# Performance work log

Hardware: AMD Instinct MI355X
Metric: run time of the kernel (lower is better)

## Reference

```python
import jax, jax.numpy as jnp
import numpy as np

K = 3  # TAGConv default number of hops
N, E = 50000, 800000
F_X, F_POS, HID, OUT = 6, 2, 64, 10


def _tagconv(x, W, b, src, dst, norm, n):
    # TAGConv: out = sum_{k=0}^{K} (A_norm^k x) @ W[k] + b
    out = x @ W[0]
    h = x
    for k in range(1, K + 1):
        # one propagate step: gather from src, weight, scatter-sum to dst
        h = jax.ops.segment_sum(norm[:, None] * h[src], dst, num_segments=n)
        out = out + h @ W[k]
    return out + b


def setup_inputs() -> dict:
    key = jax.random.key(0)
    ks = jax.random.split(key, 12)
    x = jax.random.normal(ks[0], (N, F_X), dtype=jnp.float32)
    pos = jax.random.normal(ks[1], (N, F_POS), dtype=jnp.float32)
    edge_index = jax.random.randint(ks[2], (2, E), 0, N, dtype=jnp.int64)
    edge_attr = jax.random.uniform(ks[3], (E,), dtype=jnp.float32)
    s = 0.1
    W1 = jax.random.normal(ks[4], (K + 1, F_X + F_POS, HID), dtype=jnp.float32) * s
    b1 = jnp.zeros((HID,), dtype=jnp.float32)
    W2 = jax.random.normal(ks[5], (K + 1, HID, HID), dtype=jnp.float32) * s
    b2 = jnp.zeros((HID,), dtype=jnp.float32)
    W3 = jax.random.normal(ks[6], (K + 1, HID, OUT), dtype=jnp.float32) * s
    b3 = jnp.zeros((OUT,), dtype=jnp.float32)
    return {"x": x, "pos": pos, "edge_attr": edge_attr,
            "W1": W1, "b1": b1, "W2": W2, "b2": b2, "W3": W3, "b3": b3,
            "edge_index": edge_index}


def reference(x, pos, edge_attr, W1, b1, W2, b2, W3, b3, edge_index):
    n = x.shape[0]
    src, dst = edge_index[0], edge_index[1]
    # gcn_norm (no self loops, as in TAGConv): deg over destination (col)
    deg = jax.ops.segment_sum(edge_attr, dst, num_segments=n)
    dinv = jnp.where(deg > 0, jax.lax.rsqrt(deg), jnp.zeros_like(deg))
    norm = dinv[src] * edge_attr * dinv[dst]
    h = jnp.concatenate([x, pos], axis=1)
    h = jax.nn.relu(_tagconv(h, W1, b1, src, dst, norm, n))
    # F.dropout with training=False is identity (eval reference)
    h = jax.nn.relu(_tagconv(h, W2, b2, src, dst, norm, n))
    h = _tagconv(h, W3, b3, src, dst, norm, n)
    return jax.nn.log_softmax(h, axis=1)
```

## Files before the change

### kernel.cpp

```cpp
#include <hip/hip_runtime.h>
#include <math.h>


#define NN 50000
#define EE 800000
#define HID 64
#define NOUT 10
#define CH 512

#define NB 391
#define CAP 2400
#define K1_EPB 2048

typedef __attribute__((ext_vector_type(8))) short bf16x8;
typedef __attribute__((ext_vector_type(4))) float f32x4;

__device__ __forceinline__ unsigned bf16rnd(float x) {
    unsigned u = __float_as_uint(x);
    return (u + 0x7FFFu + ((u >> 16) & 1u)) >> 16;
}
__device__ __forceinline__ unsigned packbf2(float a, float b) {
    return bf16rnd(a) | (bf16rnd(b) << 16);
}
__device__ __forceinline__ float bflo(unsigned u) { return __uint_as_float(u << 16); }
__device__ __forceinline__ float bfhi(unsigned u) { return __uint_as_float(u & 0xFFFF0000u); }

__global__ __launch_bounds__(512) void bucket_scatter_kernel(
        const int* __restrict__ src, const int* __restrict__ dst,
        const float* __restrict__ ea, int* __restrict__ cursor,
        int2* __restrict__ regions, int e) {
    __shared__ int hist[NB];
    __shared__ int base_s[NB];
    int tid = threadIdx.x;
    int e0 = blockIdx.x * K1_EPB;
    int e1 = e0 + K1_EPB; if (e1 > e) e1 = e;
    int d[4], s[4];
    float w[4];
    int cnt = 0;
    for (int i = e0 + tid; i < e1; i += 512) {
        d[cnt] = dst[i]; s[cnt] = src[i]; w[cnt] = ea[i];
        ++cnt;
    }
    for (int i = tid; i < NB; i += 512) hist[i] = 0;
    __syncthreads();
    for (int j = 0; j < cnt; ++j)
        atomicAdd(&hist[d[j] >> 7], 1);
    __syncthreads();
    for (int b = tid; b < NB; b += 512) {
        int c = hist[b];
        base_s[b] = (c > 0) ? atomicAdd(&cursor[b], c) : 0;
        hist[b] = 0;
    }
    __syncthreads();
    for (int j = 0; j < cnt; ++j) {
        int b = d[j] >> 7;
        int r = atomicAdd(&hist[b], 1);
        int pos = base_s[b] + r;
        if (pos < CAP)
            regions[(size_t)b * CAP + pos] =
                make_int2(((d[j] & 127) << 16) | s[j], __float_as_int(w[j]));
    }
}

__global__ __launch_bounds__(512) void bucket_build_kernel(
        const int* __restrict__ cursor, int2* __restrict__ regions,
        float* __restrict__ dinv, int* __restrict__ row_start, int n) {
    __shared__ int2 rec[CAP];
    __shared__ int hist[128];
    __shared__ float easum[128];
    __shared__ float dl[128];
    __shared__ int off[129];
    __shared__ int lcur[128];
    int b = blockIdx.x;
    int tid = threadIdx.x;
    int cnt = cursor[b]; if (cnt > CAP) cnt = CAP;
    size_t rb = (size_t)b * CAP;
    if (tid < 128) { hist[tid] = 0; easum[tid] = 0.f; lcur[tid] = 0; }
    __syncthreads();
    for (int i = tid; i < cnt; i += 512) {
        int2 r = regions[rb + i];
        rec[i] = r;
        int f = r.x >> 16;
        atomicAdd(&hist[f], 1);
        atomicAdd(&easum[f], __int_as_float(r.y));
    }
    __syncthreads();
    if (tid < 128) {
        int lane = tid & 63;
        int v = hist[tid];
        for (int o2 = 1; o2 < 64; o2 <<= 1) {
            int y = __shfl_up(v, o2, 64);
            if (lane >= o2) v += y;
        }
        off[tid + 1] = v;
        float s2 = easum[tid];
        dl[tid] = (s2 > 0.f) ? rsqrtf(s2) : 0.f;
    }
    __syncthreads();
    if (tid == 255) off[0] = 0;
    if (tid >= 64 && tid < 128) off[tid + 1] += off[64];
    __syncthreads();
    if (tid < 128) {
        int node = b * 128 + tid;
        if (node <= n) row_start[node] = b * CAP + off[tid];
        if (node < n)  dinv[node] = dl[tid];
    }
    __syncthreads();
    for (int i = tid; i < cnt; i += 512) {
        int2 r = rec[i];
        int f = r.x >> 16;
        int s = r.x & 0xFFFF;
        int p = atomicAdd(&lcur[f], 1);
        float w0 = __int_as_float(r.y) * dl[f];
        regions[rb + off[f] + p] = make_int2(s, __float_as_int(w0));
    }
}

__global__ __launch_bounds__(256) void pack1_kernel(const float* __restrict__ x,
                                                    const float* __restrict__ pos,
                                                    unsigned short* __restrict__ B1, int n) {
    int i = blockIdx.x * blockDim.x + threadIdx.x;
    if (i >= n) return;
    float2 a = *reinterpret_cast<const float2*>(x + (size_t)i * 6);
    float2 b = *reinterpret_cast<const float2*>(x + (size_t)i * 6 + 2);
    float2 c = *reinterpret_cast<const float2*>(x + (size_t)i * 6 + 4);
    float2 p = *reinterpret_cast<const float2*>(pos + (size_t)i * 2);
    uint4 o;
    o.x = packbf2(a.x, a.y);
    o.y = packbf2(b.x, b.y);
    o.z = packbf2(c.x, c.y);
    o.w = packbf2(p.x, p.y);
    *reinterpret_cast<uint4*>(B1 + (size_t)i * 32) = o;
}

template <int SCALE>
__global__ __launch_bounds__(256) void prop8b_kernel(const int* __restrict__ row_start,
                                                     const int* __restrict__ cursor,
                                                     int2* __restrict__ edges,
                                                     const float* __restrict__ dinv,
                                                     const unsigned short* __restrict__ Gin,
                                                     unsigned short* __restrict__ Gout, int n) {
    constexpr int TEAM = 8, NPB = 32;
    __shared__ int2 se[CH];
    int tid = threadIdx.x;
    int nb = blockIdx.x * NPB;
    int node = nb + tid / TEAM;
    int es = tid % TEAM;
    int nbEnd = (nb + NPB < n) ? (nb + NPB) : n;
    int bkt = nb >> 7;
    int cc = cursor[bkt]; if (cc > CAP) cc = CAP;
    int ce = bkt * CAP + cc;
    int blkBeg = row_start[nb];
    int blkEnd = row_start[nbEnd]; if (blkEnd > ce) blkEnd = ce;
    int beg = 0, end = 0;
    if (node < n) {
        beg = row_start[node];
        end = row_start[node + 1]; if (end > ce) end = ce;
    }
    float a0 = 0.f, a1 = 0.f, a2 = 0.f, a3 = 0.f, a4 = 0.f, a5 = 0.f, a6 = 0.f, a7 = 0.f;
    for (int base = blkBeg; base < blkEnd; base += CH) {
        int m = blkEnd - base; if (m > CH) m = CH;
        __syncthreads();
        for (int i = tid; i < m; i += 256) {
            int2 r = edges[base + i];
            if (SCALE) {
                r.y = __float_as_int(__int_as_float(r.y) * dinv[r.x]);
                edges[base + i] = r;
            }
            se[i] = r;
        }
        __syncthreads();
        int lo = (beg > base) ? (beg - base) : 0;
        int hi = ((end < base + m) ? end : (base + m)) - base;
        for (int i = lo + es; i < hi; i += TEAM) {
            int2 e = se[i];
            float w = __int_as_float(e.y);
            const uint4 v = *reinterpret_cast<const uint4*>(Gin + (size_t)e.x * 32);
            a0 += w * bflo(v.x); a1 += w * bfhi(v.x);
            a2 += w * bflo(v.y); a3 += w * bfhi(v.y);
            a4 += w * bflo(v.z); a5 += w * bfhi(v.z);
            a6 += w * bflo(v.w); a7 += w * bfhi(v.w);
        }
    }
    #pragma unroll
    for (int msk = 1; msk < TEAM; msk <<= 1) {
        a0 += __shfl_xor(a0, msk); a1 += __shfl_xor(a1, msk);
        a2 += __shfl_xor(a2, msk); a3 += __shfl_xor(a3, msk);
        a4 += __shfl_xor(a4, msk); a5 += __shfl_xor(a5, msk);
        a6 += __shfl_xor(a6, msk); a7 += __shfl_xor(a7, msk);
    }
    if (node < n && es == 0) {
        uint4 o;
        o.x = packbf2(a0, a1);
        o.y = packbf2(a2, a3);
        o.z = packbf2(a4, a5);
        o.w = packbf2(a6, a7);
        *reinterpret_cast<uint4*>(Gout + (size_t)node * 32) = o;
    }
}

template <int TPN, int ES, bool ACC>
__global__ __launch_bounds__(256) void prop_kernel(const int* __restrict__ row_start,
                                                   const int* __restrict__ cursor,
                                                   const int2* __restrict__ edges,
                                                   const float* __restrict__ hin, int in_stride,
                                                   float* __restrict__ hout, int out_stride, int n) {
    constexpr int TEAM = TPN * ES;
    constexpr int NPB = 256 / TEAM;
    __shared__ int2 se[CH];
    int tid = threadIdx.x;
    int nb = blockIdx.x * NPB;
    int node = nb + tid / TEAM;
    int t = tid % TEAM;
    int es = t / TPN;
    int lane = t % TPN;
    int nbEnd = (nb + NPB < n) ? (nb + NPB) : n;
    int bkt = nb >> 7;
    int cc = cursor[bkt]; if (cc > CAP) cc = CAP;
    int ce = bkt * CAP + cc;
    int blkBeg = row_start[nb];
    int blkEnd = row_start[nbEnd]; if (blkEnd > ce) blkEnd = ce;
    int beg = 0, end = 0;
    if (node < n) {
        beg = row_start[node];
        end = row_start[node + 1]; if (end > ce) end = ce;
    }
    float ax = 0.f, ay = 0.f, az = 0.f, aw = 0.f;
    for (int base = blkBeg; base < blkEnd; base += CH) {
        int m = blkEnd - base; if (m > CH) m = CH;
        __syncthreads();
        for (int i = tid; i < m; i += 256) se[i] = edges[base + i];
        __syncthreads();
        int lo = (beg > base) ? (beg - base) : 0;
        int hi = ((end < base + m) ? end : (base + m)) - base;
        for (int i = lo + es; i < hi; i += ES) {
            int2 e = se[i];
            float w = __int_as_float(e.y);
            const float4 v = *reinterpret_cast<const float4*>(hin + (size_t)e.x * in_stride + lane * 4);
            ax += w * v.x; ay += w * v.y; az += w * v.z; aw += w * v.w;
        }
    }
    #pragma unroll
    for (int msk = TPN; msk < TEAM; msk <<= 1) {
        ax += __shfl_xor(ax, msk);
        ay += __shfl_xor(ay, msk);
        az += __shfl_xor(az, msk);
        aw += __shfl_xor(aw, msk);
    }
    if (node < n && es == 0) {
        float4* po = reinterpret_cast<float4*>(hout + (size_t)node * out_stride + lane * 4);
        float4 r = make_float4(ax, ay, az, aw);
        if (ACC) { float4 o = *po; r.x += o.x; r.y += o.y; r.z += o.z; r.w += o.w; }
        *po = r;
    }
}

__global__ __launch_bounds__(256) void prop64b_kernel(const int* __restrict__ row_start,
                                                      const int* __restrict__ cursor,
                                                      const int2* __restrict__ edges,
                                                      const unsigned short* __restrict__ Gin,
                                                      unsigned short* __restrict__ Gout, int n) {
    constexpr int TPN = 8, ES = 4, TEAM = 32, NPB = 8;
    __shared__ int2 se[CH];
    int tid = threadIdx.x;
    int nb = blockIdx.x * NPB;
    int node = nb + tid / TEAM;
    int t = tid % TEAM;
    int es = t / TPN;
    int lane = t % TPN;
    int nbEnd = (nb + NPB < n) ? (nb + NPB) : n;
    int bkt = nb >> 7;
    int cc = cursor[bkt]; if (cc > CAP) cc = CAP;
    int ce = bkt * CAP + cc;
    int blkBeg = row_start[nb];
    int blkEnd = row_start[nbEnd]; if (blkEnd > ce) blkEnd = ce;
    int beg = 0, end = 0;
    if (node < n) {
        beg = row_start[node];
        end = row_start[node + 1]; if (end > ce) end = ce;
    }
    float a0 = 0.f, a1 = 0.f, a2 = 0.f, a3 = 0.f, a4 = 0.f, a5 = 0.f, a6 = 0.f, a7 = 0.f;
    for (int base = blkBeg; base < blkEnd; base += CH) {
        int m = blkEnd - base; if (m > CH) m = CH;
        __syncthreads();
        for (int i = tid; i < m; i += 256) se[i] = edges[base + i];
        __syncthreads();
        int lo = (beg > base) ? (beg - base) : 0;
        int hi = ((end < base + m) ? end : (base + m)) - base;
        for (int i = lo + es; i < hi; i += ES) {
            int2 e = se[i];
            float w = __int_as_float(e.y);
            const uint4 v = *reinterpret_cast<const uint4*>(Gin + (size_t)e.x * 256 + lane * 8);
            a0 += w * bflo(v.x); a1 += w * bfhi(v.x);
            a2 += w * bflo(v.y); a3 += w * bfhi(v.y);
            a4 += w * bflo(v.z); a5 += w * bfhi(v.z);
            a6 += w * bflo(v.w); a7 += w * bfhi(v.w);
        }
    }
    #pragma unroll
    for (int msk = TPN; msk < TEAM; msk <<= 1) {
        a0 += __shfl_xor(a0, msk); a1 += __shfl_xor(a1, msk);
        a2 += __shfl_xor(a2, msk); a3 += __shfl_xor(a3, msk);
        a4 += __shfl_xor(a4, msk); a5 += __shfl_xor(a5, msk);
        a6 += __shfl_xor(a6, msk); a7 += __shfl_xor(a7, msk);
    }
    if (node < n && es == 0) {
        uint4 o;
        o.x = packbf2(a0, a1);
        o.y = packbf2(a2, a3);
        o.z = packbf2(a4, a5);
        o.w = packbf2(a6, a7);
        *reinterpret_cast<uint4*>(Gout + (size_t)node * 256 + lane * 8) = o;
    }
}

__global__ __launch_bounds__(256) void prop_final_kernel(const int* __restrict__ row_start,
                                                         const int* __restrict__ cursor,
                                                         const int2* __restrict__ edges,
                                                         const float* __restrict__ hin,
                                                         const float* __restrict__ g0,
                                                         const float* __restrict__ b3,
                                                         float* __restrict__ out, int n) {
    constexpr int TPN = 4, ES = 2, TEAM = 8, NPB = 32;
    __shared__ int2 se[CH];
    int tid = threadIdx.x;
    int nb = blockIdx.x * NPB;
    int node = nb + tid / TEAM;
    int t = tid % TEAM;
    int es = t / TPN;
    int lane = t % TPN;
    int nbEnd = (nb + NPB < n) ? (nb + NPB) : n;
    int bkt = nb >> 7;
    int cc = cursor[bkt]; if (cc > CAP) cc = CAP;
    int ce = bkt * CAP + cc;
    int blkBeg = row_start[nb];
    int blkEnd = row_start[nbEnd]; if (blkEnd > ce) blkEnd = ce;
    int beg = 0, end = 0;
    if (node < n) {
        beg = row_start[node];
        end = row_start[node + 1]; if (end > ce) end = ce;
    }
    float ax = 0.f, ay = 0.f, az = 0.f, aw = 0.f;
    for (int base = blkBeg; base < blkEnd; base += CH) {
        int m = blkEnd - base; if (m > CH) m = CH;
        __syncthreads();
        for (int i = tid; i < m; i += 256) se[i] = edges[base + i];
        __syncthreads();
        int lo = (beg > base) ? (beg - base) : 0;
        int hi = ((end < base + m) ? end : (base + m)) - base;
        for (int i = lo + es; i < hi; i += ES) {
            int2 e = se[i];
            float w = __int_as_float(e.y);
            const float4 v = *reinterpret_cast<const float4*>(hin + (size_t)e.x * 64 + lane * 4);
            ax += w * v.x; ay += w * v.y; az += w * v.z; aw += w * v.w;
        }
    }
    ax += __shfl_xor(ax, TPN);
    ay += __shfl_xor(ay, TPN);
    az += __shfl_xor(az, TPN);
    aw += __shfl_xor(aw, TPN);
    if (node < n && es == 0) {
        const float4 g = *reinterpret_cast<const float4*>(g0 + (size_t)node * 64 + lane * 4);
        float vv[4] = {ax + g.x, ay + g.y, az + g.z, aw + g.w};
        int c0 = lane * 4;
        float mloc = -1e30f;
        #pragma unroll
        for (int c = 0; c < 4; ++c) {
            int col = c0 + c;
            if (col < NOUT) { vv[c] += b3[col]; mloc = fmaxf(mloc, vv[c]); }
        }
        float mo = fmaxf(mloc, __shfl_xor(mloc, 1));
        mo = fmaxf(mo, __shfl_xor(mo, 2));
        float sl = 0.f;
        #pragma unroll
        for (int c = 0; c < 4; ++c) {
            int col = c0 + c;
            if (col < NOUT) sl += __expf(vv[c] - mo);
        }
        sl += __shfl_xor(sl, 1);
        sl += __shfl_xor(sl, 2);
        float ls = __logf(sl);
        #pragma unroll
        for (int c = 0; c < 4; ++c) {
            int col = c0 + c;
            if (col < NOUT) out[(size_t)node * NOUT + col] = vv[c] - mo - ls;
        }
    }
}

__global__ __launch_bounds__(256) void mm1_kernel(const unsigned short* __restrict__ B1,
                                                  const float* __restrict__ W1,
                                                  const float* __restrict__ b1,
                                                  unsigned short* __restrict__ G, int n) {
    __shared__ unsigned short w1s[2048];
    __shared__ unsigned short hs[64 * 64];
    int tid = threadIdx.x;
    int wave = tid >> 6;
    int lane = tid & 63;
    int nodeBase = blockIdx.x * 64;

    {
        int l = tid & 63;
        int t = tid >> 6;
        int k0 = (l >> 4) << 3;
        int col = t * 16 + (l & 15);
        unsigned short tmp[8];
        #pragma unroll
        for (int j = 0; j < 8; ++j)
            tmp[j] = (unsigned short)bf16rnd(W1[(size_t)(k0 + j) * 64 + col]);
        *reinterpret_cast<uint4*>(w1s + tid * 8) = *reinterpret_cast<const uint4*>(tmp);
    }
    __syncthreads();

    int arow = nodeBase + wave * 16 + (lane & 15);
    bf16x8 a = {};
    if (arow < n)
        a = *reinterpret_cast<const bf16x8*>(B1 + (size_t)arow * 32 + ((lane >> 4) << 3));
    const unsigned short* wb = w1s + lane * 8;
    f32x4 acc0 = {0.f, 0.f, 0.f, 0.f}, acc1 = {0.f, 0.f, 0.f, 0.f};
    f32x4 acc2 = {0.f, 0.f, 0.f, 0.f}, acc3 = {0.f, 0.f, 0.f, 0.f};
    acc0 = __builtin_amdgcn_mfma_f32_16x16x32_bf16(a, *reinterpret_cast<const bf16x8*>(wb),        acc0, 0, 0, 0);
    acc1 = __builtin_amdgcn_mfma_f32_16x16x32_bf16(a, *reinterpret_cast<const bf16x8*>(wb + 512),  acc1, 0, 0, 0);
    acc2 = __builtin_amdgcn_mfma_f32_16x16x32_bf16(a, *reinterpret_cast<const bf16x8*>(wb + 1024), acc2, 0, 0, 0);
    acc3 = __builtin_amdgcn_mfma_f32_16x16x32_bf16(a, *reinterpret_cast<const bf16x8*>(wb + 1536), acc3, 0, 0, 0);

    {
        int c = lane & 15;
        int rbase = wave * 16 + (lane >> 4) * 4;
        f32x4 accs[4] = {acc0, acc1, acc2, acc3};
        #pragma unroll
        for (int t = 0; t < 4; ++t) {
            int col = t * 16 + c;
            float bb = b1[col];
            #pragma unroll
            for (int r = 0; r < 4; ++r) {
                float v = accs[t][r] + bb;
                hs[(rbase + r) * 64 + col] = (unsigned short)bf16rnd(v > 0.f ? v : 0.f);
            }
        }
    }
    __syncthreads();
    for (int i = tid; i < 512; i += 256) {
        int nd = i >> 3, ch = i & 7;
        int node = nodeBase + nd;
        if (node < n)
            *reinterpret_cast<uint4*>(G + (size_t)node * 256 + ch * 8) =
                *reinterpret_cast<const uint4*>(hs + nd * 64 + ch * 8);
    }
}

__global__ __launch_bounds__(256) void mm23_kernel(const unsigned short* __restrict__ G,
                                                   const float* __restrict__ W2,
                                                   const float* __restrict__ b2,
                                                   const float* __restrict__ W3,
                                                   float* __restrict__ T, int n) {
    constexpr int HP = 68;
    __shared__ __align__(16) char smem[33792];
    unsigned short* w2s = (unsigned short*)smem;
    float* HsT = (float*)smem;
    float* Ws  = (float*)(smem + 64 * HP * 4);
    int tid = threadIdx.x;
    int wave = tid >> 6;
    int lane = tid & 63;
    int nodeBase = blockIdx.x * 64;

    for (int slot = tid; slot < 2048; slot += 256) {
        int l = slot & 63;
        int s = (slot >> 6) & 7;
        int t = slot >> 9;
        int k0 = s * 32 + ((l >> 4) << 3);
        int col = t * 16 + (l & 15);
        unsigned short tmp[8];
        #pragma unroll
        for (int j = 0; j < 8; ++j)
            tmp[j] = (unsigned short)bf16rnd(W2[(size_t)(k0 + j) * 64 + col]);
        *reinterpret_cast<uint4*>(w2s + slot * 8) = *reinterpret_cast<const uint4*>(tmp);
    }
    __syncthreads();

    int arow = nodeBase + wave * 16 + (lane & 15);
    bool aval = (arow < n);
    const unsigned short* arp = G + (size_t)arow * 256 + ((lane >> 4) << 3);
    f32x4 acc0 = {0.f, 0.f, 0.f, 0.f}, acc1 = {0.f, 0.f, 0.f, 0.f};
    f32x4 acc2 = {0.f, 0.f, 0.f, 0.f}, acc3 = {0.f, 0.f, 0.f, 0.f};
    #pragma unroll
    for (int s = 0; s < 8; ++s) {
        bf16x8 a = {};
        if (aval) a = *reinterpret_cast<const bf16x8*>(arp + s * 32);
        const unsigned short* wb = w2s + ((size_t)s * 64 + lane) * 8;
        bf16x8 bf0 = *reinterpret_cast<const bf16x8*>(wb);
        bf16x8 bf1 = *reinterpret_cast<const bf16x8*>(wb + 4096);
        bf16x8 bf2 = *reinterpret_cast<const bf16x8*>(wb + 8192);
        bf16x8 bf3 = *reinterpret_cast<const bf16x8*>(wb + 12288);
        acc0 = __builtin_amdgcn_mfma_f32_16x16x32_bf16(a, bf0, acc0, 0, 0, 0);
        acc1 = __builtin_amdgcn_mfma_f32_16x16x32_bf16(a, bf1, acc1, 0, 0, 0);
        acc2 = __builtin_amdgcn_mfma_f32_16x16x32_bf16(a, bf2, acc2, 0, 0, 0);
        acc3 = __builtin_amdgcn_mfma_f32_16x16x32_bf16(a, bf3, acc3, 0, 0, 0);
    }
    __syncthreads();

    {
        int c = lane & 15;
        int rbase = wave * 16 + (lane >> 4) * 4;
        f32x4 accs[4] = {acc0, acc1, acc2, acc3};
        #pragma unroll
        for (int t = 0; t < 4; ++t) {
            int col = t * 16 + c;
            float bb = b2[col];
            #pragma unroll
            for (int r = 0; r < 4; ++r) {
                float v = accs[t][r] + bb;
                HsT[col * HP + rbase + r] = v > 0.f ? v : 0.f;
            }
        }
    }
    for (int i = tid; i < 64 * 64; i += 256) {
        int r = i >> 6, c2 = i & 63;
        int k = c2 >> 4, j = c2 & 15;
        Ws[i] = (j < NOUT) ? W3[((size_t)k * 64 + r) * NOUT + j] : 0.f;
    }
    __syncthreads();

    int ndq = tid >> 4;
    int f4  = tid & 15;
    float4 t0 = make_float4(0.f, 0.f, 0.f, 0.f);
    float4 t1 = make_float4(0.f, 0.f, 0.f, 0.f);
    float4 t2 = make_float4(0.f, 0.f, 0.f, 0.f);
    float4 t3 = make_float4(0.f, 0.f, 0.f, 0.f);
    #pragma unroll 8
    for (int k = 0; k < 64; ++k) {
        const float4 hq = *reinterpret_cast<const float4*>(&HsT[k * HP + ndq * 4]);
        const float4 wq = *reinterpret_cast<const float4*>(&Ws[k * 64 + f4 * 4]);
        t0.x += hq.x * wq.x; t0.y += hq.x * wq.y; t0.z += hq.x * wq.z; t0.w += hq.x * wq.w;
        t1.x += hq.y * wq.x; t1.y += hq.y * wq.y; t1.z += hq.y * wq.z; t1.w += hq.y * wq.w;
        t2.x += hq.z * wq.x; t2.y += hq.z * wq.y; t2.z += hq.z * wq.z; t2.w += hq.z * wq.w;
        t3.x += hq.w * wq.x; t3.y += hq.w * wq.y; t3.z += hq.w * wq.z; t3.w += hq.w * wq.w;
    }
    float4 ts[4] = {t0, t1, t2, t3};
    #pragma unroll
    for (int i = 0; i < 4; ++i) {
        int node = nodeBase + ndq * 4 + i;
        if (node < n)
            *reinterpret_cast<float4*>(T + (size_t)node * 64 + f4 * 4) = ts[i];
    }
}

extern "C" void kernel_launch(void* const* d_in, const int* in_sizes, int n_in,
                              void* d_out, int out_size, void* d_ws, size_t ws_size,
                              hipStream_t stream) {
    const float* x   = (const float*)d_in[0];
    const float* pos = (const float*)d_in[1];
    const float* ea  = (const float*)d_in[2];
    const float* W1  = (const float*)d_in[3];
    const float* b1  = (const float*)d_in[4];
    const float* W2  = (const float*)d_in[5];
    const float* b2  = (const float*)d_in[6];
    const float* W3  = (const float*)d_in[7];
    const float* b3  = (const float*)d_in[8];
    const int* eidx  = (const int*)d_in[9];
    const int* src = eidx;
    const int* dst = eidx + EE;
    float* outp = (float*)d_out;

    size_t off = 0;
    char* base = (char*)d_ws;
    auto alloc = [&](size_t bytes) -> void* {
        void* p = base + off;
        off += (bytes + 255) & ~(size_t)255;
        return p;
    };
    int*   cursor    = (int*)alloc(NB * 4);
    int*   row_start = (int*)alloc((NN + 1) * 4);
    float* dinv      = (float*)alloc(NN * 4);
    int2*  edges     = (int2*)alloc((size_t)NB * CAP * 8);
    unsigned short* G  = (unsigned short*)alloc((size_t)NN * 256 * 2);
    unsigned short* B1 = (unsigned short*)alloc((size_t)NN * 32 * 2);
    float* T         = (float*)alloc((size_t)NN * 64 * 4);
    (void)ws_size;

    const int B = 256;
    const int gN = (NN + B - 1) / B;
    const int gK1 = (EE + K1_EPB - 1) / K1_EPB;
    const int gMM2 = (NN + 63) / 64;
    const int gP32 = (NN + 31) / 32;
    const int gP8  = (NN + 7) / 8;

    hipMemsetAsync(cursor, 0, NB * 4, stream);

    bucket_scatter_kernel<<<gK1, 512, 0, stream>>>(src, dst, ea, cursor, edges, EE);
    bucket_build_kernel<<<NB, 512, 0, stream>>>(cursor, edges, dinv, row_start, NN);

    pack1_kernel<<<gN, B, 0, stream>>>(x, pos, B1, NN);
    prop8b_kernel<1><<<gP32, B, 0, stream>>>(row_start, cursor, edges, dinv, B1,      B1 + 8,  NN);
    prop8b_kernel<0><<<gP32, B, 0, stream>>>(row_start, cursor, edges, dinv, B1 + 8,  B1 + 16, NN);
    prop8b_kernel<0><<<gP32, B, 0, stream>>>(row_start, cursor, edges, dinv, B1 + 16, B1 + 24, NN);
    mm1_kernel<<<gMM2, B, 0, stream>>>(B1, W1, b1, G, NN);

    prop64b_kernel<<<gP8, B, 0, stream>>>(row_start, cursor, edges, G,       G + 64,  NN);
    prop64b_kernel<<<gP8, B, 0, stream>>>(row_start, cursor, edges, G + 64,  G + 128, NN);
    prop64b_kernel<<<gP8, B, 0, stream>>>(row_start, cursor, edges, G + 128, G + 192, NN);
    mm23_kernel<<<gMM2, B, 0, stream>>>(G, W2, b2, W3, T, NN);

    prop_kernel<4, 2, true><<<gP32, B, 0, stream>>>(row_start, cursor, edges, T + 48, 64, T + 32, 64, NN);
    prop_kernel<4, 2, true><<<gP32, B, 0, stream>>>(row_start, cursor, edges, T + 32, 64, T + 16, 64, NN);
    prop_final_kernel<<<gP32, B, 0, stream>>>(row_start, cursor, edges, T + 16, T, b3, outp, NN);
}
```

Baseline: 273.7 us.

## Compress edge records to 32-bit (16-bit src + fp16 weight) and retune propagation teams

Edge records change from int2 (src, fp32 weight) to a packed 32-bit word holding a 16-bit source index and an fp16 weight, written to a separate buffer by the build kernel. This halves edge-list traffic in all nine propagation passes and lets the shared-memory chunk size double to 1024. The 10-wide propagation kernels switch to 4 edge-slices per node with 16 nodes per block. The cost is reduced weight precision from fp16 rounding, including the rescaled weights in the first pass. The 16-bit index also only works because N is below 65536.

```diff
diff --git a/kernel.cpp b/kernel.cpp
--- a/kernel.cpp
+++ b/kernel.cpp
@@ -1,4 +1,5 @@
 #include <hip/hip_runtime.h>
+#include <hip/hip_fp16.h>
 #include <math.h>
 
 
@@ -6,7 +7,7 @@
 #define EE 800000
 #define HID 64
 #define NOUT 10
-#define CH 512
+#define CH 1024
 
 #define NB 391
 #define CAP 2400
@@ -24,6 +25,15 @@
 }
 __device__ __forceinline__ float bflo(unsigned u) { return __uint_as_float(u << 16); }
 __device__ __forceinline__ float bfhi(unsigned u) { return __uint_as_float(u & 0xFFFF0000u); }
+__device__ __forceinline__ unsigned f16b(float x) {
+    __half h = __float2half_rn(x);
+    return (unsigned)*reinterpret_cast<unsigned short*>(&h);
+}
+__device__ __forceinline__ float f16f(unsigned u) {
+    unsigned short us = (unsigned short)u;
+    __half h = *reinterpret_cast<__half*>(&us);
+    return __half2float(h);
+}
 
 __global__ __launch_bounds__(512) void bucket_scatter_kernel(
         const int* __restrict__ src, const int* __restrict__ dst,
@@ -63,7 +73,8 @@
 }
 
 __global__ __launch_bounds__(512) void bucket_build_kernel(
-        const int* __restrict__ cursor, int2* __restrict__ regions,
+        const int* __restrict__ cursor, const int2* __restrict__ regions,
+        unsigned* __restrict__ erec,
         float* __restrict__ dinv, int* __restrict__ row_start, int n) {
     __shared__ int2 rec[CAP];
     __shared__ int hist[128];
@@ -109,10 +120,10 @@
     for (int i = tid; i < cnt; i += 512) {
         int2 r = rec[i];
         int f = r.x >> 16;
-        int s = r.x & 0xFFFF;
+        unsigned s = (unsigned)(r.x & 0xFFFF);
         int p = atomicAdd(&lcur[f], 1);
         float w0 = __int_as_float(r.y) * dl[f];
-        regions[rb + off[f] + p] = make_int2(s, __float_as_int(w0));
+        erec[rb + off[f] + p] = s | (f16b(w0) << 16);
     }
 }
 
@@ -136,12 +147,12 @@
 template <int SCALE>
 __global__ __launch_bounds__(256) void prop8b_kernel(const int* __restrict__ row_start,
                                                      const int* __restrict__ cursor,
-                                                     int2* __restrict__ edges,
+                                                     unsigned* __restrict__ erec,
                                                      const float* __restrict__ dinv,
                                                      const unsigned short* __restrict__ Gin,
                                                      unsigned short* __restrict__ Gout, int n) {
     constexpr int TEAM = 8, NPB = 32;
-    __shared__ int2 se[CH];
+    __shared__ unsigned se[CH];
     int tid = threadIdx.x;
     int nb = blockIdx.x * NPB;
     int node = nb + tid / TEAM;
@@ -162,10 +173,11 @@
         int m = blkEnd - base; if (m > CH) m = CH;
         __syncthreads();
         for (int i = tid; i < m; i += 256) {
-            int2 r = edges[base + i];
+            unsigned r = erec[base + i];
             if (SCALE) {
-                r.y = __float_as_int(__int_as_float(r.y) * dinv[r.x]);
-                edges[base + i] = r;
+                float w = f16f(r >> 16) * dinv[r & 0xFFFF];
+                r = (r & 0xFFFFu) | (f16b(w) << 16);
+                erec[base + i] = r;
             }
             se[i] = r;
         }
@@ -173,9 +185,9 @@
         int lo = (beg > base) ? (beg - base) : 0;
         int hi = ((end < base + m) ? end : (base + m)) - base;
         for (int i = lo + es; i < hi; i += TEAM) {
-            int2 e = se[i];
-            float w = __int_as_float(e.y);
-            const uint4 v = *reinterpret_cast<const uint4*>(Gin + (size_t)e.x * 32);
+            unsigned e = se[i];
+            float w = f16f(e >> 16);
+            const uint4 v = *reinterpret_cast<const uint4*>(Gin + (size_t)(e & 0xFFFF) * 32);
             a0 += w * bflo(v.x); a1 += w * bfhi(v.x);
             a2 += w * bflo(v.y); a3 += w * bfhi(v.y);
             a4 += w * bflo(v.z); a5 += w * bfhi(v.z);
@@ -202,12 +214,12 @@
 template <int TPN, int ES, bool ACC>
 __global__ __launch_bounds__(256) void prop_kernel(const int* __restrict__ row_start,
                                                    const int* __restrict__ cursor,
-                                                   const int2* __restrict__ edges,
+                                                   const unsigned* __restrict__ erec,
                                                    const float* __restrict__ hin, int in_stride,
                                                    float* __restrict__ hout, int out_stride, int n) {
     constexpr int TEAM = TPN * ES;
     constexpr int NPB = 256 / TEAM;
-    __shared__ int2 se[CH];
+    __shared__ unsigned se[CH];
     int tid = threadIdx.x;
     int nb = blockIdx.x * NPB;
     int node = nb + tid / TEAM;
@@ -229,14 +241,14 @@
     for (int base = blkBeg; base < blkEnd; base += CH) {
         int m = blkEnd - base; if (m > CH) m = CH;
         __syncthreads();
-        for (int i = tid; i < m; i += 256) se[i] = edges[base + i];
+        for (int i = tid; i < m; i += 256) se[i] = erec[base + i];
         __syncthreads();
         int lo = (beg > base) ? (beg - base) : 0;
         int hi = ((end < base + m) ? end : (base + m)) - base;
         for (int i = lo + es; i < hi; i += ES) {
-            int2 e = se[i];
-            float w = __int_as_float(e.y);
-            const float4 v = *reinterpret_cast<const float4*>(hin + (size_t)e.x * in_stride + lane * 4);
+            unsigned e = se[i];
+            float w = f16f(e >> 16);
+            const float4 v = *reinterpret_cast<const float4*>(hin + (size_t)(e & 0xFFFF) * in_stride + lane * 4);
             ax += w * v.x; ay += w * v.y; az += w * v.z; aw += w * v.w;
         }
     }
@@ -257,11 +269,11 @@
 
 __global__ __launch_bounds__(256) void prop64b_kernel(const int* __restrict__ row_start,
                                                       const int* __restrict__ cursor,
-                                                      const int2* __restrict__ edges,
+                                                      const unsigned* __restrict__ erec,
                                                       const unsigned short* __restrict__ Gin,
                                                       unsigned short* __restrict__ Gout, int n) {
     constexpr int TPN = 8, ES = 4, TEAM = 32, NPB = 8;
-    __shared__ int2 se[CH];
+    __shared__ unsigned se[CH];
     int tid = threadIdx.x;
     int nb = blockIdx.x * NPB;
     int node = nb + tid / TEAM;
@@ -283,14 +295,14 @@
     for (int base = blkBeg; base < blkEnd; base += CH) {
         int m = blkEnd - base; if (m > CH) m = CH;
         __syncthreads();
-        for (int i = tid; i < m; i += 256) se[i] = edges[base + i];
+        for (int i = tid; i < m; i += 256) se[i] = erec[base + i];
         __syncthreads();
         int lo = (beg > base) ? (beg - base) : 0;
         int hi = ((end < base + m) ? end : (base + m)) - base;
         for (int i = lo + es; i < hi; i += ES) {
-            int2 e = se[i];
-            float w = __int_as_float(e.y);
-            const uint4 v = *reinterpret_cast<const uint4*>(Gin + (size_t)e.x * 256 + lane * 8);
+            unsigned e = se[i];
+            float w = f16f(e >> 16);
+            const uint4 v = *reinterpret_cast<const uint4*>(Gin + (size_t)(e & 0xFFFF) * 256 + lane * 8);
             a0 += w * bflo(v.x); a1 += w * bfhi(v.x);
             a2 += w * bflo(v.y); a3 += w * bfhi(v.y);
             a4 += w * bflo(v.z); a5 += w * bfhi(v.z);
@@ -316,13 +328,13 @@
 
 __global__ __launch_bounds__(256) void prop_final_kernel(const int* __restrict__ row_start,
                                                          const int* __restrict__ cursor,
-                                                         const int2* __restrict__ edges,
+                                                         const unsigned* __restrict__ erec,
                                                          const float* __restrict__ hin,
                                                          const float* __restrict__ g0,
                                                          const float* __restrict__ b3,
                                                          float* __restrict__ out, int n) {
-    constexpr int TPN = 4, ES = 2, TEAM = 8, NPB = 32;
-    __shared__ int2 se[CH];
+    constexpr int TPN = 4, ES = 4, TEAM = 16, NPB = 16;
+    __shared__ unsigned se[CH];
     int tid = threadIdx.x;
     int nb = blockIdx.x * NPB;
     int node = nb + tid / TEAM;
@@ -344,21 +356,24 @@
     for (int base = blkBeg; base < blkEnd; base += CH) {
         int m = blkEnd - base; if (m > CH) m = CH;
         __syncthreads();
-        for (int i = tid; i < m; i += 256) se[i] = edges[base + i];
+        for (int i = tid; i < m; i += 256) se[i] = erec[base + i];
         __syncthreads();
         int lo = (beg > base) ? (beg - base) : 0;
         int hi = ((end < base + m) ? end : (base + m)) - base;
         for (int i = lo + es; i < hi; i += ES) {
-            int2 e = se[i];
-            float w = __int_as_float(e.y);
-            const float4 v = *reinterpret_cast<const float4*>(hin + (size_t)e.x * 64 + lane * 4);
+            unsigned e = se[i];
+            float w = f16f(e >> 16);
+            const float4 v = *reinterpret_cast<const float4*>(hin + (size_t)(e & 0xFFFF) * 64 + lane * 4);
             ax += w * v.x; ay += w * v.y; az += w * v.z; aw += w * v.w;
         }
     }
-    ax += __shfl_xor(ax, TPN);
-    ay += __shfl_xor(ay, TPN);
-    az += __shfl_xor(az, TPN);
-    aw += __shfl_xor(aw, TPN);
+    #pragma unroll
+    for (int msk = TPN; msk < TEAM; msk <<= 1) {
+        ax += __shfl_xor(ax, msk);
+        ay += __shfl_xor(ay, msk);
+        az += __shfl_xor(az, msk);
+        aw += __shfl_xor(aw, msk);
+    }
     if (node < n && es == 0) {
         const float4 g = *reinterpret_cast<const float4*>(g0 + (size_t)node * 64 + lane * 4);
         float vv[4] = {ax + g.x, ay + g.y, az + g.z, aw + g.w};
@@ -572,7 +587,8 @@
     int*   cursor    = (int*)alloc(NB * 4);
     int*   row_start = (int*)alloc((NN + 1) * 4);
     float* dinv      = (float*)alloc(NN * 4);
-    int2*  edges     = (int2*)alloc((size_t)NB * CAP * 8);
+    int2*  regions   = (int2*)alloc((size_t)NB * CAP * 8);
+    unsigned* erec   = (unsigned*)alloc((size_t)NB * CAP * 4);
     unsigned short* G  = (unsigned short*)alloc((size_t)NN * 256 * 2);
     unsigned short* B1 = (unsigned short*)alloc((size_t)NN * 32 * 2);
     float* T         = (float*)alloc((size_t)NN * 64 * 4);
@@ -583,25 +599,26 @@
     const int gK1 = (EE + K1_EPB - 1) / K1_EPB;
     const int gMM2 = (NN + 63) / 64;
     const int gP32 = (NN + 31) / 32;
+    const int gP16 = (NN + 15) / 16;
     const int gP8  = (NN + 7) / 8;
 
     hipMemsetAsync(cursor, 0, NB * 4, stream);
 
-    bucket_scatter_kernel<<<gK1, 512, 0, stream>>>(src, dst, ea, cursor, edges, EE);
-    bucket_build_kernel<<<NB, 512, 0, stream>>>(cursor, edges, dinv, row_start, NN);
+    bucket_scatter_kernel<<<gK1, 512, 0, stream>>>(src, dst, ea, cursor, regions, EE);
+    bucket_build_kernel<<<NB, 512, 0, stream>>>(cursor, regions, erec, dinv, row_start, NN);
 
     pack1_kernel<<<gN, B, 0, stream>>>(x, pos, B1, NN);
-    prop8b_kernel<1><<<gP32, B, 0, stream>>>(row_start, cursor, edges, dinv, B1,      B1 + 8,  NN);
-    prop8b_kernel<0><<<gP32, B, 0, stream>>>(row_start, cursor, edges, dinv, B1 + 8,  B1 + 16, NN);
-    prop8b_kernel<0><<<gP32, B, 0, stream>>>(row_start, cursor, edges, dinv, B1 + 16, B1 + 24, NN);
+    prop8b_kernel<1><<<gP32, B, 0, stream>>>(row_start, cursor, erec, dinv, B1,      B1 + 8,  NN);
+    prop8b_kernel<0><<<gP32, B, 0, stream>>>(row_start, cursor, erec, dinv, B1 + 8,  B1 + 16, NN);
+    prop8b_kernel<0><<<gP32, B, 0, stream>>>(row_start, cursor, erec, dinv, B1 + 16, B1 + 24, NN);
     mm1_kernel<<<gMM2, B, 0, stream>>>(B1, W1, b1, G, NN);
 
-    prop64b_kernel<<<gP8, B, 0, stream>>>(row_start, cursor, edges, G,       G + 64,  NN);
-    prop64b_kernel<<<gP8, B, 0, stream>>>(row_start, cursor, edges, G + 64,  G + 128, NN);
-    prop64b_kernel<<<gP8, B, 0, stream>>>(row_start, cursor, edges, G + 128, G + 192, NN);
+    prop64b_kernel<<<gP8, B, 0, stream>>>(row_start, cursor, erec, G,       G + 64,  NN);
+    prop64b_kernel<<<gP8, B, 0, stream>>>(row_start, cursor, erec, G + 64,  G + 128, NN);
+    prop64b_kernel<<<gP8, B, 0, stream>>>(row_start, cursor, erec, G + 128, G + 192, NN);
     mm23_kernel<<<gMM2, B, 0, stream>>>(G, W2, b2, W3, T, NN);
 
-    prop_kernel<4, 2, true><<<gP32, B, 0, stream>>>(row_start, cursor, edges, T + 48, 64, T + 32, 64, NN);
-    prop_kernel<4, 2, true><<<gP32, B, 0, stream>>>(row_start, cursor, edges, T + 32, 64, T + 16, 64, NN);
-    prop_final_kernel<<<gP32, B, 0, stream>>>(row_start, cursor, edges, T + 16, T, b3, outp, NN);
-}
+    prop_kernel<4, 4, true><<<gP16, B, 0, stream>>>(row_start, cursor, erec, T + 48, 64, T + 32, 64, NN);
+    prop_kernel<4, 4, true><<<gP16, B, 0, stream>>>(row_start, cursor, erec, T + 32, 64, T + 16, 64, NN);
+    prop_final_kernel<<<gP16, B, 0, stream>>>(row_start, cursor, erec, T + 16, T, b3, outp, NN);
+}
```

New measurement: 262.1 us. 4.2% less time.
